# Kernel tuning notes

Measured on AMD Instinct MI355X. Metric: run time of the kernel, lower is better.

Reference implementation:

```python
import jax, jax.numpy as jnp
import numpy as np

Re = 0.001
DT = 0.01
UB = -1.0
PAD = ((0, 0), (0, 0), (1, 1), (1, 1), (1, 1))


def _conv(x, w, stride=1):
    return jax.lax.conv_general_dilated(
        x, w, (stride, stride, stride), 'VALID',
        dimension_numbers=('NCDHW', 'OIDHW', 'NCDHW'))


def _pad_zero(x):
    return jnp.pad(x, PAD)


def _pad_edge(x):
    return jnp.pad(x, PAD, mode='edge')


def bc_u(u):
    # zero halo everywhere, inlet value ub on the low-x face
    return _pad_zero(u).at[..., 0].set(UB)


bc_v = _pad_zero
bc_w = _pad_zero
bc_p = _pad_edge   # Neumann (replicate) for pressure
bc_k = _pad_edge
bc_cw = _pad_zero  # Dirichlet-0 for coarse corrections


def prol(x):
    # nearest-neighbor upsample x2 in z, y, x
    x = jnp.repeat(x, 2, axis=2)
    x = jnp.repeat(x, 2, axis=3)
    return jnp.repeat(x, 2, axis=4)


def solid_body(u, v, w, sigma):
    s = 1.0 + DT * sigma
    return u / s, v / s, w / s


def pg_vector(uu, vv, ww, u, v, w, w_diff):
    # k fields are ones; padded versions go through BC
    one = jnp.ones_like(u)
    k_uu = bc_k(one)
    k_u = 0.5 * (one * _conv(uu, w_diff) + _conv(uu * k_uu, w_diff) - u * _conv(k_uu, w_diff))
    k_v = 0.5 * (one * _conv(vv, w_diff) + _conv(vv * k_uu, w_diff) - v * _conv(k_uu, w_diff))
    k_w = 0.5 * (one * _conv(ww, w_diff) + _conv(ww * k_uu, w_diff) - w * _conv(k_uu, w_diff))
    return k_u, k_v, k_w


def f_cycle_mg(uu, vv, ww, p, pp, wA, w_x, w_y, w_z, w_res, iteration, nlevel):
    diag = wA[0, 0, 1, 1, 1]
    b = -(_conv(uu, w_x) + _conv(vv, w_y) + _conv(ww, w_z)) / DT
    nz, ny, nx = p.shape[2:]
    f = 2 ** (nlevel - 2)  # coarsening factor of the coarsest level
    for _ in range(iteration):
        w = jnp.zeros((1, 1, nz // f, ny // f, nx // f), dtype=p.dtype)
        r = _conv(pp, wA) - b
        r_s = [r]
        for _i in range(1, nlevel - 1):
            r = _conv(r, w_res, stride=2)
            r_s.append(r)
        for i in reversed(range(1, nlevel - 1)):
            ww_pad = bc_cw(w)
            w = w - _conv(ww_pad, wA) / diag + r_s[i] / diag
            w = prol(w)
        p = p - w
        p = p - _conv(pp, wA) / diag + b / diag
        pp = bc_p(p)
    return p, w, r


def reference(values_u, values_v, values_w, values_p, sigma,
              wA, w_diff, w_x, w_y, w_z, w_res, iteration, nlevel):
    u, v, w, p = values_u, values_v, values_w, values_p
    u, v, w = solid_body(u, v, w, sigma)
    uu, vv, ww, pp = bc_u(u), bc_v(v), bc_w(w), bc_p(p)

    k_u, k_v, k_w = pg_vector(uu, vv, ww, u, v, w, w_diff)
    b_u = u + 0.5 * (Re * k_u * DT - u * _conv(uu, w_x) * DT - v * _conv(uu, w_y) * DT - w * _conv(uu, w_z) * DT) - _conv(pp, w_x) * DT
    b_v = v + 0.5 * (Re * k_v * DT - u * _conv(vv, w_x) * DT - v * _conv(vv, w_y) * DT - w * _conv(vv, w_z) * DT) - _conv(pp, w_y) * DT
    b_w = w + 0.5 * (Re * k_w * DT - u * _conv(ww, w_x) * DT - v * _conv(ww, w_y) * DT - w * _conv(ww, w_z) * DT) - _conv(pp, w_z) * DT
    b_u, b_v, b_w = solid_body(b_u, b_v, b_w, sigma)
    b_uu, b_vv, b_ww = bc_u(b_u), bc_v(b_v), bc_w(b_w)

    k_u, k_v, k_w = pg_vector(b_uu, b_vv, b_ww, b_u, b_v, b_w, w_diff)
    u = u + Re * k_u * DT - b_u * _conv(b_uu, w_x) * DT - b_v * _conv(b_uu, w_y) * DT - b_w * _conv(b_uu, w_z) * DT - _conv(pp, w_x) * DT
    v = v + Re * k_v * DT - b_u * _conv(b_vv, w_x) * DT - b_v * _conv(b_vv, w_y) * DT - b_w * _conv(b_vv, w_z) * DT - _conv(pp, w_y) * DT
    w = w + Re * k_w * DT - b_u * _conv(b_ww, w_x) * DT - b_v * _conv(b_ww, w_y) * DT - b_w * _conv(b_ww, w_z) * DT - _conv(pp, w_z) * DT
    u, v, w = solid_body(u, v, w, sigma)
    uu, vv, ww = bc_u(u), bc_v(v), bc_w(w)

    p, w_mg, r = f_cycle_mg(uu, vv, ww, p, pp, wA, w_x, w_y, w_z, w_res, iteration, nlevel)
    pp = bc_p(p)
    u = u - _conv(pp, w_x) * DT
    v = v - _conv(pp, w_y) * DT
    w = w - _conv(pp, w_z) * DT
    u, v, w = solid_body(u, v, w, sigma)
    return u, v, w, p, w_mg, r


def setup_inputs() -> dict:
    key = jax.random.key(0)
    ks = jax.random.split(key, 5)
    NZ, NY, NX = 64, 128, 256
    shape = (1, 1, NZ, NY, NX)

    # 7-point Laplacian for A and diff
    lap = np.zeros((1, 1, 3, 3, 3), np.float32)
    lap[0, 0, 1, 1, 1] = -6.0
    for d, i in [(2, 0), (2, 2), (3, 0), (3, 2), (4, 0), (4, 2)]:
        idx = [0, 0, 1, 1, 1]
        idx[d] = i
        lap[tuple(idx)] = 1.0
    # central differences
    wx = np.zeros((1, 1, 3, 3, 3), np.float32); wx[0, 0, 1, 1, 0] = -0.5; wx[0, 0, 1, 1, 2] = 0.5
    wy = np.zeros((1, 1, 3, 3, 3), np.float32); wy[0, 0, 1, 0, 1] = -0.5; wy[0, 0, 1, 2, 1] = 0.5
    wz = np.zeros((1, 1, 3, 3, 3), np.float32); wz[0, 0, 0, 1, 1] = -0.5; wz[0, 0, 2, 1, 1] = 0.5
    wres = np.full((1, 1, 2, 2, 2), 0.125, np.float32)

    return {
        'values_u': 0.1 * jax.random.normal(ks[0], shape, jnp.float32),
        'values_v': 0.1 * jax.random.normal(ks[1], shape, jnp.float32),
        'values_w': 0.1 * jax.random.normal(ks[2], shape, jnp.float32),
        'values_p': 0.1 * jax.random.normal(ks[3], shape, jnp.float32),
        'sigma': jax.random.uniform(ks[4], shape, jnp.float32),
        'wA': jnp.asarray(lap),
        'w_diff': jnp.asarray(lap),
        'w_x': jnp.asarray(wx),
        'w_y': jnp.asarray(wy),
        'w_z': jnp.asarray(wz),
        'w_res': jnp.asarray(wres),
        'iteration': 2,
        'nlevel': 6,
    }
```

## Files before the change

### kernel.cpp

```cpp
#include <hip/hip_runtime.h>


constexpr int NZ = 64, NY = 128, NX = 256;
constexpr int NTOT = NZ * NY * NX;
constexpr float DT  = 0.01f;
constexpr float RE  = 0.001f;
constexpr float UBC = -1.0f;
constexpr float DIAG = -6.0f;
constexpr float SIXTH = 1.0f / 6.0f;

__device__ __forceinline__ int idx3(int z, int y, int x) {
    return (z * NY + y) * NX + x;
}

union F4 { float4 v; float f[4]; };

__device__ __forceinline__ float4 ld4(const float* __restrict__ f, int z, int y, int x0) {
    return *reinterpret_cast<const float4*>(&f[idx3(z, y, x0)]);
}
__device__ __forceinline__ void st4(float* __restrict__ f, int c, const F4& a) {
    *reinterpret_cast<float4*>(&f[c]) = a.v;
}

__device__ __forceinline__ void row0(const float* __restrict__ f, int z, int y, int x0,
                                     bool ok, float o[4]) {
    if (ok) { F4 a; a.v = ld4(f, z, y, x0);
        #pragma unroll
        for (int i = 0; i < 4; i++) o[i] = a.f[i];
    } else {
        #pragma unroll
        for (int i = 0; i < 4; i++) o[i] = 0.f;
    }
}
__device__ __forceinline__ void row3s(const float* __restrict__ u, const float* __restrict__ v,
                                      const float* __restrict__ w, const float* __restrict__ sg,
                                      int z, int y, int x0, bool ok,
                                      float uo[4], float vo[4], float wo[4]) {
    if (ok) {
        F4 a, b, c, s;
        a.v = ld4(u, z, y, x0); b.v = ld4(v, z, y, x0);
        c.v = ld4(w, z, y, x0); s.v = ld4(sg, z, y, x0);
        #pragma unroll
        for (int i = 0; i < 4; i++) {
            float iv = 1.f / (1.f + DT * s.f[i]);
            uo[i] = a.f[i] * iv; vo[i] = b.f[i] * iv; wo[i] = c.f[i] * iv;
        }
    } else {
        #pragma unroll
        for (int i = 0; i < 4; i++) { uo[i] = vo[i] = wo[i] = 0.f; }
    }
}

__device__ __forceinline__ float ld_p_s(const float* __restrict__ f, int z, int y, int x) {
    x = x < 0 ? 0 : (x > NX - 1 ? NX - 1 : x);
    y = y < 0 ? 0 : (y > NY - 1 ? NY - 1 : y);
    z = z < 0 ? 0 : (z > NZ - 1 ? NZ - 1 : z);
    return f[idx3(z, y, x)];
}

__global__ __launch_bounds__(256) void k_predict(
    const float* __restrict__ u, const float* __restrict__ v, const float* __restrict__ w,
    const float* __restrict__ p, const float* __restrict__ sg,
    float* __restrict__ bu, float* __restrict__ bv, float* __restrict__ bw) {
    int tx = threadIdx.x, y = blockIdx.x * 4 + threadIdx.y, z = blockIdx.y;
    int x0 = tx << 2, c = idx3(z, y, x0);

    F4 sc; sc.v = ld4(sg, z, y, x0);
    F4 u4, v4, w4; u4.v = ld4(u, z, y, x0); v4.v = ld4(v, z, y, x0); w4.v = ld4(w, z, y, x0);
    float inv[4], uc[4], vc[4], wc[4];
    #pragma unroll
    for (int i = 0; i < 4; i++) {
        inv[i] = 1.f / (1.f + DT * sc.f[i]);
        uc[i] = u4.f[i] * inv[i]; vc[i] = v4.f[i] * inv[i]; wc[i] = w4.f[i] * inv[i];
    }
    float uym[4], vym[4], wym[4], uyp[4], vyp[4], wyp[4];
    float uzm[4], vzm[4], wzm[4], uzp[4], vzp[4], wzp[4];
    row3s(u, v, w, sg, z, y - 1, x0, y > 0,      uym, vym, wym);
    row3s(u, v, w, sg, z, y + 1, x0, y < NY - 1, uyp, vyp, wyp);
    row3s(u, v, w, sg, z - 1, y, x0, z > 0,      uzm, vzm, wzm);
    row3s(u, v, w, sg, z + 1, y, x0, z < NZ - 1, uzp, vzp, wzp);

    float uxmS, vxmS, wxmS, uxpS, vxpS, wxpS;
    if (tx > 0) { float iv = 1.f / (1.f + DT * sg[c - 1]);
        uxmS = u[c - 1] * iv; vxmS = v[c - 1] * iv; wxmS = w[c - 1] * iv; }
    else { uxmS = UBC; vxmS = 0.f; wxmS = 0.f; }
    if (tx < 63) { float iv = 1.f / (1.f + DT * sg[c + 4]);
        uxpS = u[c + 4] * iv; vxpS = v[c + 4] * iv; wxpS = w[c + 4] * iv; }
    else { uxpS = vxpS = wxpS = 0.f; }

    F4 pc, pym, pyp, pzm, pzp;
    pc.v  = ld4(p, z, y, x0);
    pym.v = ld4(p, z, y > 0 ? y - 1 : 0, x0);
    pyp.v = ld4(p, z, y < NY - 1 ? y + 1 : y, x0);
    pzm.v = ld4(p, z > 0 ? z - 1 : 0, y, x0);
    pzp.v = ld4(p, z < NZ - 1 ? z + 1 : z, y, x0);
    float pxmS = tx ? p[c - 1] : pc.f[0];
    float pxpS = (tx < 63) ? p[c + 4] : pc.f[3];

    F4 obu, obv, obw;
    #pragma unroll
    for (int i = 0; i < 4; i++) {
        float uxm = i ? uc[i - 1] : uxmS, uxp = (i < 3) ? uc[i + 1] : uxpS;
        float vxm = i ? vc[i - 1] : vxmS, vxp = (i < 3) ? vc[i + 1] : vxpS;
        float wxm = i ? wc[i - 1] : wxmS, wxp = (i < 3) ? wc[i + 1] : wxpS;
        float pxm = i ? pc.f[i - 1] : pxmS, pxp = (i < 3) ? pc.f[i + 1] : pxpS;
        float dpx = 0.5f * (pxp - pxm);
        float dpy = 0.5f * (pyp.f[i] - pym.f[i]);
        float dpz = 0.5f * (pzp.f[i] - pzm.f[i]);
        float lap_u = uxm + uxp + uym[i] + uyp[i] + uzm[i] + uzp[i] - 6.f * uc[i];
        float lap_v = vxm + vxp + vym[i] + vyp[i] + vzm[i] + vzp[i] - 6.f * vc[i];
        float lap_w = wxm + wxp + wym[i] + wyp[i] + wzm[i] + wzp[i] - 6.f * wc[i];
        float bun = uc[i] + 0.5f * (RE * lap_u * DT
                    - uc[i] * (0.5f * (uxp - uxm)) * DT
                    - vc[i] * (0.5f * (uyp[i] - uym[i])) * DT
                    - wc[i] * (0.5f * (uzp[i] - uzm[i])) * DT) - dpx * DT;
        float bvn = vc[i] + 0.5f * (RE * lap_v * DT
                    - uc[i] * (0.5f * (vxp - vxm)) * DT
                    - vc[i] * (0.5f * (vyp[i] - vym[i])) * DT
                    - wc[i] * (0.5f * (vzp[i] - vzm[i])) * DT) - dpy * DT;
        float bwn = wc[i] + 0.5f * (RE * lap_w * DT
                    - uc[i] * (0.5f * (wxp - wxm)) * DT
                    - vc[i] * (0.5f * (wyp[i] - wym[i])) * DT
                    - wc[i] * (0.5f * (wzp[i] - wzm[i])) * DT) - dpz * DT;
        obu.f[i] = bun * inv[i];
        obv.f[i] = bvn * inv[i];
        obw.f[i] = bwn * inv[i];
    }
    st4(bu, c, obu); st4(bv, c, obv); st4(bw, c, obw);
}

__global__ __launch_bounds__(256) void k_correct(
    const float* __restrict__ u, const float* __restrict__ v, const float* __restrict__ w,
    const float* __restrict__ sg,
    const float* __restrict__ bu, const float* __restrict__ bv, const float* __restrict__ bw,
    const float* __restrict__ p,
    float* __restrict__ u2, float* __restrict__ v2, float* __restrict__ w2) {
    int tx = threadIdx.x, y = blockIdx.x * 4 + threadIdx.y, z = blockIdx.y;
    int x0 = tx << 2, c = idx3(z, y, x0);

    F4 sc; sc.v = ld4(sg, z, y, x0);
    F4 u4, v4, w4; u4.v = ld4(u, z, y, x0); v4.v = ld4(v, z, y, x0); w4.v = ld4(w, z, y, x0);
    F4 buc, bvc, bwc; buc.v = ld4(bu, z, y, x0); bvc.v = ld4(bv, z, y, x0); bwc.v = ld4(bw, z, y, x0);

    float uym[4], vym[4], wym[4], uyp[4], vyp[4], wyp[4];
    float uzm[4], vzm[4], wzm[4], uzp[4], vzp[4], wzp[4];
    row0(bu, z, y - 1, x0, y > 0, uym);      row0(bv, z, y - 1, x0, y > 0, vym);
    row0(bw, z, y - 1, x0, y > 0, wym);
    row0(bu, z, y + 1, x0, y < NY - 1, uyp); row0(bv, z, y + 1, x0, y < NY - 1, vyp);
    row0(bw, z, y + 1, x0, y < NY - 1, wyp);
    row0(bu, z - 1, y, x0, z > 0, uzm);      row0(bv, z - 1, y, x0, z > 0, vzm);
    row0(bw, z - 1, y, x0, z > 0, wzm);
    row0(bu, z + 1, y, x0, z < NZ - 1, uzp); row0(bv, z + 1, y, x0, z < NZ - 1, vzp);
    row0(bw, z + 1, y, x0, z < NZ - 1, wzp);

    float uxmS = tx ? bu[c - 1] : UBC,  uxpS = (tx < 63) ? bu[c + 4] : 0.f;
    float vxmS = tx ? bv[c - 1] : 0.f,  vxpS = (tx < 63) ? bv[c + 4] : 0.f;
    float wxmS = tx ? bw[c - 1] : 0.f,  wxpS = (tx < 63) ? bw[c + 4] : 0.f;

    F4 pc, pym, pyp, pzm, pzp;
    pc.v  = ld4(p, z, y, x0);
    pym.v = ld4(p, z, y > 0 ? y - 1 : 0, x0);
    pyp.v = ld4(p, z, y < NY - 1 ? y + 1 : y, x0);
    pzm.v = ld4(p, z > 0 ? z - 1 : 0, y, x0);
    pzp.v = ld4(p, z < NZ - 1 ? z + 1 : z, y, x0);
    float pxmS = tx ? p[c - 1] : pc.f[0];
    float pxpS = (tx < 63) ? p[c + 4] : pc.f[3];

    F4 ou, ov, ow;
    #pragma unroll
    for (int i = 0; i < 4; i++) {
        float inv = 1.f / (1.f + DT * sc.f[i]);
        float u1c = u4.f[i] * inv, v1c = v4.f[i] * inv, w1c = w4.f[i] * inv;
        float uxm = i ? buc.f[i - 1] : uxmS, uxp = (i < 3) ? buc.f[i + 1] : uxpS;
        float vxm = i ? bvc.f[i - 1] : vxmS, vxp = (i < 3) ? bvc.f[i + 1] : vxpS;
        float wxm = i ? bwc.f[i - 1] : wxmS, wxp = (i < 3) ? bwc.f[i + 1] : wxpS;
        float pxm = i ? pc.f[i - 1] : pxmS, pxp = (i < 3) ? pc.f[i + 1] : pxpS;
        float dpx = 0.5f * (pxp - pxm);
        float dpy = 0.5f * (pyp.f[i] - pym.f[i]);
        float dpz = 0.5f * (pzp.f[i] - pzm.f[i]);
        float lap_u = uxm + uxp + uym[i] + uyp[i] + uzm[i] + uzp[i] - 6.f * buc.f[i];
        float lap_v = vxm + vxp + vym[i] + vyp[i] + vzm[i] + vzp[i] - 6.f * bvc.f[i];
        float lap_w = wxm + wxp + wym[i] + wyp[i] + wzm[i] + wzp[i] - 6.f * bwc.f[i];
        float un = u1c + RE * lap_u * DT
                   - buc.f[i] * (0.5f * (uxp - uxm)) * DT
                   - bvc.f[i] * (0.5f * (uyp[i] - uym[i])) * DT
                   - bwc.f[i] * (0.5f * (uzp[i] - uzm[i])) * DT - dpx * DT;
        float vn = v1c + RE * lap_v * DT
                   - buc.f[i] * (0.5f * (vxp - vxm)) * DT
                   - bvc.f[i] * (0.5f * (vyp[i] - vym[i])) * DT
                   - bwc.f[i] * (0.5f * (vzp[i] - vzm[i])) * DT - dpy * DT;
        float wn = w1c + RE * lap_w * DT
                   - buc.f[i] * (0.5f * (wxp - wxm)) * DT
                   - bvc.f[i] * (0.5f * (wyp[i] - wym[i])) * DT
                   - bwc.f[i] * (0.5f * (wzp[i] - wzm[i])) * DT - dpz * DT;
        ou.f[i] = un * inv; ov.f[i] = vn * inv; ow.f[i] = wn * inv;
    }
    st4(u2, c, ou); st4(v2, c, ov); st4(w2, c, ow);
}

__global__ __launch_bounds__(256) void k_divresid(
    const float* __restrict__ u2, const float* __restrict__ v2, const float* __restrict__ w2,
    const float* __restrict__ p, float* __restrict__ r0) {
    int tx = threadIdx.x, y = blockIdx.x * 4 + threadIdx.y, z = blockIdx.y;
    int x0 = tx << 2, c = idx3(z, y, x0);

    F4 uc; uc.v = ld4(u2, z, y, x0);
    float uxmS = tx ? u2[c - 1] : UBC, uxpS = (tx < 63) ? u2[c + 4] : 0.f;
    float vym[4], vyp[4], wzm[4], wzp[4];
    row0(v2, z, y - 1, x0, y > 0, vym);
    row0(v2, z, y + 1, x0, y < NY - 1, vyp);
    row0(w2, z - 1, y, x0, z > 0, wzm);
    row0(w2, z + 1, y, x0, z < NZ - 1, wzp);

    F4 pc, pym, pyp, pzm, pzp;
    pc.v  = ld4(p, z, y, x0);
    pym.v = ld4(p, z, y > 0 ? y - 1 : 0, x0);
    pyp.v = ld4(p, z, y < NY - 1 ? y + 1 : y, x0);
    pzm.v = ld4(p, z > 0 ? z - 1 : 0, y, x0);
    pzp.v = ld4(p, z < NZ - 1 ? z + 1 : z, y, x0);
    float pxmS = tx ? p[c - 1] : pc.f[0];
    float pxpS = (tx < 63) ? p[c + 4] : pc.f[3];

    F4 o;
    #pragma unroll
    for (int i = 0; i < 4; i++) {
        float uxm = i ? uc.f[i - 1] : uxmS, uxp = (i < 3) ? uc.f[i + 1] : uxpS;
        float bval = -(0.5f * (uxp - uxm) + 0.5f * (vyp[i] - vym[i])
                       + 0.5f * (wzp[i] - wzm[i])) / DT;
        float pxm = i ? pc.f[i - 1] : pxmS, pxp = (i < 3) ? pc.f[i + 1] : pxpS;
        float lap = pxm + pxp + pym.f[i] + pyp.f[i] + pzm.f[i] + pzp.f[i] - 6.f * pc.f[i];
        o.f[i] = lap - bval;
    }
    st4(r0, c, o);
}

__global__ __launch_bounds__(512) void k_rescdown(const float* __restrict__ rf,
    float* __restrict__ r1, float* __restrict__ r2, float* __restrict__ r3,
    float* __restrict__ r4) {
    __shared__ float l1[8][16][32];
    __shared__ float l2[4][8][16];
    __shared__ float l3[2][4][8];
    int tid = threadIdx.x;
    int bx = blockIdx.x, by = blockIdx.y, bz = blockIdx.z;
    int lx = tid & 31, ly = (tid >> 5) & 15;
    int x1 = bx * 32 + lx, y1 = by * 16 + ly;
    #pragma unroll
    for (int lz = 0; lz < 8; lz++) {
        int z1 = bz * 8 + lz;
        const float* b0 = &rf[idx3(2 * z1, 2 * y1, 2 * x1)];
        float2 a  = *reinterpret_cast<const float2*>(b0);
        float2 bq = *reinterpret_cast<const float2*>(b0 + NX);
        float2 cq = *reinterpret_cast<const float2*>(b0 + NY * NX);
        float2 dq = *reinterpret_cast<const float2*>(b0 + NY * NX + NX);
        float val = 0.125f * (a.x + a.y + bq.x + bq.y + cq.x + cq.y + dq.x + dq.y);
        l1[lz][ly][lx] = val;
        r1[((z1 * 64) + y1) * 128 + x1] = val;
    }
    __syncthreads();
    {
        int tx2 = tid & 15, ty2 = (tid >> 4) & 7, tz2 = tid >> 7;
        float s = l1[2*tz2][2*ty2][2*tx2]     + l1[2*tz2][2*ty2][2*tx2+1]
                + l1[2*tz2][2*ty2+1][2*tx2]   + l1[2*tz2][2*ty2+1][2*tx2+1]
                + l1[2*tz2+1][2*ty2][2*tx2]   + l1[2*tz2+1][2*ty2][2*tx2+1]
                + l1[2*tz2+1][2*ty2+1][2*tx2] + l1[2*tz2+1][2*ty2+1][2*tx2+1];
        float val = 0.125f * s;
        l2[tz2][ty2][tx2] = val;
        int x2 = bx * 16 + tx2, y2 = by * 8 + ty2, z2 = bz * 4 + tz2;
        r2[((z2 * 32) + y2) * 64 + x2] = val;
    }
    __syncthreads();
    if (tid < 64) {
        int tx3 = tid & 7, ty3 = (tid >> 3) & 3, tz3 = tid >> 5;
        float s = l2[2*tz3][2*ty3][2*tx3]     + l2[2*tz3][2*ty3][2*tx3+1]
                + l2[2*tz3][2*ty3+1][2*tx3]   + l2[2*tz3][2*ty3+1][2*tx3+1]
                + l2[2*tz3+1][2*ty3][2*tx3]   + l2[2*tz3+1][2*ty3][2*tx3+1]
                + l2[2*tz3+1][2*ty3+1][2*tx3] + l2[2*tz3+1][2*ty3+1][2*tx3+1];
        float val = 0.125f * s;
        l3[tz3][ty3][tx3] = val;
        int x3 = bx * 8 + tx3, y3 = by * 4 + ty3, z3 = bz * 2 + tz3;
        r3[((z3 * 16) + y3) * 32 + x3] = val;
    }
    __syncthreads();
    if (tid < 8) {
        int tx4 = tid & 3, ty4 = tid >> 2;
        float s = l3[0][2*ty4][2*tx4]   + l3[0][2*ty4][2*tx4+1]
                + l3[0][2*ty4+1][2*tx4] + l3[0][2*ty4+1][2*tx4+1]
                + l3[1][2*ty4][2*tx4]   + l3[1][2*ty4][2*tx4+1]
                + l3[1][2*ty4+1][2*tx4] + l3[1][2*ty4+1][2*tx4+1];
        int x4 = bx * 4 + tx4, y4 = by * 2 + ty4, z4 = bz;
        r4[((z4 * 8) + y4) * 16 + x4] = 0.125f * s;
    }
}

__device__ __forceinline__ float a4p(const float* __restrict__ r4, int z3, int y3, int x3) {
    if ((unsigned)z3 >= 8u || (unsigned)y3 >= 16u || (unsigned)x3 >= 32u) return 0.f;
    return r4[(((z3 >> 1) * 8) + (y3 >> 1)) * 16 + (x3 >> 1)] / DIAG;
}

__global__ __launch_bounds__(512) void k_cup(const float* __restrict__ r4,
    const float* __restrict__ r3, const float* __restrict__ r2, float* __restrict__ C) {
    __shared__ float Bl[4][6][10];
    int tid = threadIdx.x;
    int bx = blockIdx.x, by = blockIdx.y, bz = blockIdx.z;
    int Bz0 = bz * 2 - 1, By0 = by * 4 - 1, Bx0 = bx * 8 - 1;
    if (tid < 240) {
        int lx = tid % 10, ly = (tid / 10) % 6, lz = tid / 60;
        int z3 = Bz0 + lz, y3 = By0 + ly, x3 = Bx0 + lx;
        float val = 0.f;
        if ((unsigned)z3 < 8u && (unsigned)y3 < 16u && (unsigned)x3 < 32u) {
            float wcn = r4[(((z3 >> 1) * 8) + (y3 >> 1)) * 16 + (x3 >> 1)] / DIAG;
            float lap = a4p(r4, z3 - 1, y3, x3) + a4p(r4, z3 + 1, y3, x3)
                      + a4p(r4, z3, y3 - 1, x3) + a4p(r4, z3, y3 + 1, x3)
                      + a4p(r4, z3, y3, x3 - 1) + a4p(r4, z3, y3, x3 + 1) - 6.f * wcn;
            val = wcn - lap / DIAG + r3[((z3 * 16) + y3) * 32 + x3] / DIAG;
        }
        Bl[lz][ly][lx] = val;
    }
    __syncthreads();
    int tx = tid & 15, ty = (tid >> 4) & 7, tz = tid >> 7;
    int x2 = bx * 16 + tx, y2 = by * 8 + ty, z2 = bz * 4 + tz;
    auto bl = [&](int z, int y, int x) -> float {
        if ((unsigned)z >= 16u || (unsigned)y >= 32u || (unsigned)x >= 64u) return 0.f;
        return Bl[(z >> 1) - Bz0][(y >> 1) - By0][(x >> 1) - Bx0];
    };
    float wB = Bl[(z2 >> 1) - Bz0][(y2 >> 1) - By0][(x2 >> 1) - Bx0];
    float lap = bl(z2 - 1, y2, x2) + bl(z2 + 1, y2, x2)
              + bl(z2, y2 - 1, x2) + bl(z2, y2 + 1, x2)
              + bl(z2, y2, x2 - 1) + bl(z2, y2, x2 + 1) - 6.f * wB;
    int i = ((z2 * 32) + y2) * 64 + x2;
    C[i] = wB - lap / DIAG + r2[i] / DIAG;
}

__device__ __forceinline__ float wprol(const float* __restrict__ Wc,
                                       int zz, int yy, int xx, int Z, int Y, int X) {
    if ((unsigned)xx >= (unsigned)X || (unsigned)yy >= (unsigned)Y || (unsigned)zz >= (unsigned)Z) return 0.f;
    return Wc[(((zz >> 1) * (Y >> 1)) + (yy >> 1)) * (X >> 1) + (xx >> 1)];
}
__global__ void k_up(const float* __restrict__ Wc, const float* __restrict__ r,
                     float* __restrict__ out) {
    int X = blockDim.x, Y = gridDim.x, Z = gridDim.y;
    int x = threadIdx.x, y = blockIdx.x, z = blockIdx.y;
    float wcn = Wc[(((z >> 1) * (Y >> 1)) + (y >> 1)) * (X >> 1) + (x >> 1)];
    float lap = wprol(Wc, z - 1, y, x, Z, Y, X) + wprol(Wc, z + 1, y, x, Z, Y, X)
              + wprol(Wc, z, y - 1, x, Z, Y, X) + wprol(Wc, z, y + 1, x, Z, Y, X)
              + wprol(Wc, z, y, x - 1, Z, Y, X) + wprol(Wc, z, y, x + 1, Z, Y, X)
              - 6.f * wcn;
    int i = (z * Y + y) * X + x;
    out[i] = wcn - lap / DIAG + r[i] / DIAG;
}

__global__ __launch_bounds__(256) void k_pup_resid(
    const float* __restrict__ pin, const float* __restrict__ D0,
    const float* __restrict__ r0, float* __restrict__ p1, float* __restrict__ r1res) {
    int tx = threadIdx.x, y = blockIdx.x * 4 + threadIdx.y, z = blockIdx.y;
    int x0 = tx << 2, c = idx3(z, y, x0);
    int cz = z >> 1, cy = y >> 1, cx0 = tx << 1;

    const float* Drow = &D0[(cz * 64 + cy) * 128];
    float cr[4];
    cr[1] = Drow[cx0]; cr[2] = Drow[cx0 + 1];
    cr[0] = tx ? Drow[cx0 - 1] : cr[1];
    cr[3] = (tx < 63) ? Drow[cx0 + 2] : cr[2];
    int cym = y ? (y - 1) >> 1 : 0, cyp = (y < NY - 1) ? (y + 1) >> 1 : cy;
    int czm = z ? (z - 1) >> 1 : 0, czp = (z < NZ - 1) ? (z + 1) >> 1 : cz;
    float2 dym = *reinterpret_cast<const float2*>(&D0[(cz * 64 + cym) * 128 + cx0]);
    float2 dyp = *reinterpret_cast<const float2*>(&D0[(cz * 64 + cyp) * 128 + cx0]);
    float2 dzm = *reinterpret_cast<const float2*>(&D0[(czm * 64 + cy) * 128 + cx0]);
    float2 dzp = *reinterpret_cast<const float2*>(&D0[(czp * 64 + cy) * 128 + cx0]);

    F4 rc, rym, ryp, rzm, rzp, pin4;
    rc.v  = ld4(r0, z, y, x0);
    rym.v = ld4(r0, z, y > 0 ? y - 1 : 0, x0);
    ryp.v = ld4(r0, z, y < NY - 1 ? y + 1 : y, x0);
    rzm.v = ld4(r0, z > 0 ? z - 1 : 0, y, x0);
    rzp.v = ld4(r0, z < NZ - 1 ? z + 1 : z, y, x0);
    pin4.v = ld4(pin, z, y, x0);
    float rxmS = tx ? r0[c - 1] : rc.f[0];
    float rxpS = (tx < 63) ? r0[c + 4] : rc.f[3];

    F4 op1, ores;
    #pragma unroll
    for (int i = 0; i < 4; i++) {
        float Dc  = cr[1 + (i >> 1)];
        float Dxm = (i == 0) ? cr[0] : cr[1 + ((i - 1) >> 1)];
        float Dxp = (i == 3) ? cr[3] : cr[1 + ((i + 1) >> 1)];
        float Dym = (i < 2) ? dym.x : dym.y;
        float Dyp = (i < 2) ? dyp.x : dyp.y;
        float Dzm = (i < 2) ? dzm.x : dzm.y;
        float Dzp = (i < 2) ? dzp.x : dzp.y;
        float lapD = Dxm + Dxp + Dym + Dyp + Dzm + Dzp - 6.f * Dc;
        float rxm = i ? rc.f[i - 1] : rxmS, rxp = (i < 3) ? rc.f[i + 1] : rxpS;
        float lapR = rxm + rxp + rym.f[i] + ryp.f[i] + rzm.f[i] + rzp.f[i] - 6.f * rc.f[i];
        op1.f[i]  = pin4.f[i] - Dc + rc.f[i] * SIXTH;
        ores.f[i] = rc.f[i] - lapD + lapR * SIXTH;
    }
    st4(p1, c, op1); st4(r1res, c, ores);
}

__global__ __launch_bounds__(256) void k_pup2(
    const float* __restrict__ D1, const float* __restrict__ r1res,
    float* __restrict__ pIO, float* __restrict__ wmg) {
    int tx = threadIdx.x, y = blockIdx.x * 4 + threadIdx.y, z = blockIdx.y;
    int x0 = tx << 2, c = idx3(z, y, x0);
    int cz = z >> 1, cy = y >> 1, cx0 = tx << 1;
    float2 d2 = *reinterpret_cast<const float2*>(&D1[(cz * 64 + cy) * 128 + cx0]);
    F4 rr, pp; rr.v = ld4(r1res, z, y, x0); pp.v = ld4(pIO, z, y, x0);
    F4 op, ow;
    #pragma unroll
    for (int i = 0; i < 4; i++) {
        float wv = (i < 2) ? d2.x : d2.y;
        op.f[i] = pp.f[i] - wv + rr.f[i] * SIXTH;
        ow.f[i] = wv;
    }
    st4(pIO, c, op); st4(wmg, c, ow);
}

__global__ __launch_bounds__(256) void k_final(
    const float* __restrict__ p,
    const float* __restrict__ u2, const float* __restrict__ v2, const float* __restrict__ w2,
    const float* __restrict__ sg,
    float* __restrict__ uo, float* __restrict__ vo, float* __restrict__ wo) {
    int tx = threadIdx.x, y = blockIdx.x * 4 + threadIdx.y, z = blockIdx.y;
    int x0 = tx << 2, c = idx3(z, y, x0);
    F4 pc, pym, pyp, pzm, pzp;
    pc.v  = ld4(p, z, y, x0);
    pym.v = ld4(p, z, y > 0 ? y - 1 : 0, x0);
    pyp.v = ld4(p, z, y < NY - 1 ? y + 1 : y, x0);
    pzm.v = ld4(p, z > 0 ? z - 1 : 0, y, x0);
    pzp.v = ld4(p, z < NZ - 1 ? z + 1 : z, y, x0);
    float pxmS = tx ? p[c - 1] : pc.f[0];
    float pxpS = (tx < 63) ? p[c + 4] : pc.f[3];
    F4 sc; sc.v = ld4(sg, z, y, x0);
    F4 a, b, cc; a.v = ld4(u2, z, y, x0); b.v = ld4(v2, z, y, x0); cc.v = ld4(w2, z, y, x0);
    F4 ou, ov, ow;
    #pragma unroll
    for (int i = 0; i < 4; i++) {
        float pxm = i ? pc.f[i - 1] : pxmS, pxp = (i < 3) ? pc.f[i + 1] : pxpS;
        float inv = 1.f / (1.f + DT * sc.f[i]);
        ou.f[i] = (a.f[i]  - 0.5f * (pxp - pxm) * DT) * inv;
        ov.f[i] = (b.f[i]  - 0.5f * (pyp.f[i] - pym.f[i]) * DT) * inv;
        ow.f[i] = (cc.f[i] - 0.5f * (pzp.f[i] - pzm.f[i]) * DT) * inv;
    }
    st4(uo, c, ou); st4(vo, c, ov); st4(wo, c, ow);
}

extern "C" void kernel_launch(void* const* d_in, const int* in_sizes, int n_in,
                              void* d_out, int out_size, void* d_ws, size_t ws_size,
                              hipStream_t stream) {
    const float* in_u  = (const float*)d_in[0];
    const float* in_v  = (const float*)d_in[1];
    const float* in_w  = (const float*)d_in[2];
    const float* in_p  = (const float*)d_in[3];
    const float* in_sg = (const float*)d_in[4];

    float* out   = (float*)d_out;
    float* O_u   = out;
    float* O_v   = out + (size_t)NTOT;
    float* O_w   = out + (size_t)2 * NTOT;
    float* O_p   = out + (size_t)3 * NTOT;
    float* O_wmg = out + (size_t)4 * NTOT;
    float* O_r   = out + (size_t)5 * NTOT;

    float* ws  = (float*)d_ws;
    float* A0  = ws;
    float* A1  = ws + (size_t)NTOT;
    float* A2  = ws + (size_t)2 * NTOT;
    float* r1  = ws + (size_t)3 * NTOT;
    float* r2  = r1 + 262144;
    float* r3  = r2 + 32768;
    float* r4w = r3 + 4096;
    float* Cw  = r4w + 512;
    float* Dw  = Cw + 32768;

    dim3 gF(NY / 4, NZ);
    dim3 bF(64, 4);
    dim3 gC(4, 4, 4);

    k_predict  <<<gF, bF, 0, stream>>>(in_u, in_v, in_w, in_p, in_sg, O_u, O_v, O_w);
    k_correct  <<<gF, bF, 0, stream>>>(in_u, in_v, in_w, in_sg, O_u, O_v, O_w, in_p, A0, A1, A2);
    k_divresid <<<gF, bF, 0, stream>>>(A0, A1, A2, in_p, O_wmg );

    k_rescdown <<<gC, dim3(512), 0, stream>>>(O_wmg, r1, r2, r3, r4w);
    k_cup      <<<gC, dim3(512), 0, stream>>>(r4w, r3, r2, Cw);
    k_up       <<<dim3(64, 32), dim3(128), 0, stream>>>(Cw, r1, Dw);
    k_pup_resid<<<gF, bF, 0, stream>>>(in_p, Dw, O_wmg, O_p , O_u );

    k_rescdown <<<gC, dim3(512), 0, stream>>>(O_u, r1, r2, r3, O_r);
    k_cup      <<<gC, dim3(512), 0, stream>>>(O_r, r3, r2, Cw);
    k_up       <<<dim3(64, 32), dim3(128), 0, stream>>>(Cw, r1, Dw);
    k_pup2     <<<gF, bF, 0, stream>>>(Dw, O_u , O_p , O_wmg );

    k_final    <<<gF, bF, 0, stream>>>(O_p, A0, A1, A2, in_sg, O_u, O_v, O_w);
}
```

Baseline: 101.9 us.

## Fuse predictor into corrector, restriction into residual kernels, merge coarse up-sweeps

Predictor and corrector become one kernel that recomputes the predicted velocity for the center and its six neighbour rows instead of writing and rereading it, with the x-edge neighbours handled per point. The first restriction level moves into the residual kernels through a shared-memory 2x2x2 average, and the two coarse up-sweep kernels merge into one that holds the intermediate level in shared memory. This cuts kernel launches and full-grid memory traffic, at the price of redundant predictor arithmetic and many extra neighbour loads in the fused momentum kernel.

New measurement: 191.7 us. 1.88x slower.

```diff
diff --git a/kernel.cpp b/kernel.cpp
--- a/kernel.cpp
+++ b/kernel.cpp
@@ -22,14 +22,18 @@
     *reinterpret_cast<float4*>(&f[c]) = a.v;
 }
 
+__device__ __forceinline__ void zero4(float o[4]) {
+    #pragma unroll
+    for (int i = 0; i < 4; i++) o[i] = 0.f;
+}
+
 __device__ __forceinline__ void row0(const float* __restrict__ f, int z, int y, int x0,
                                      bool ok, float o[4]) {
     if (ok) { F4 a; a.v = ld4(f, z, y, x0);
         #pragma unroll
         for (int i = 0; i < 4; i++) o[i] = a.f[i];
     } else {
-        #pragma unroll
-        for (int i = 0; i < 4; i++) o[i] = 0.f;
+        zero4(o);
     }
 }
 __device__ __forceinline__ void row3s(const float* __restrict__ u, const float* __restrict__ v,
@@ -46,25 +50,15 @@
             uo[i] = a.f[i] * iv; vo[i] = b.f[i] * iv; wo[i] = c.f[i] * iv;
         }
     } else {
-        #pragma unroll
-        for (int i = 0; i < 4; i++) { uo[i] = vo[i] = wo[i] = 0.f; }
-    }
-}
-
-__device__ __forceinline__ float ld_p_s(const float* __restrict__ f, int z, int y, int x) {
-    x = x < 0 ? 0 : (x > NX - 1 ? NX - 1 : x);
-    y = y < 0 ? 0 : (y > NY - 1 ? NY - 1 : y);
-    z = z < 0 ? 0 : (z > NZ - 1 ? NZ - 1 : z);
-    return f[idx3(z, y, x)];
-}
-
-__global__ __launch_bounds__(256) void k_predict(
+        zero4(uo); zero4(vo); zero4(wo);
+    }
+}
+
+__device__ __forceinline__ void bu_row4(
     const float* __restrict__ u, const float* __restrict__ v, const float* __restrict__ w,
     const float* __restrict__ p, const float* __restrict__ sg,
-    float* __restrict__ bu, float* __restrict__ bv, float* __restrict__ bw) {
-    int tx = threadIdx.x, y = blockIdx.x * 4 + threadIdx.y, z = blockIdx.y;
+    int z, int y, int tx, float obu[4], float obv[4], float obw[4]) {
     int x0 = tx << 2, c = idx3(z, y, x0);
-
     F4 sc; sc.v = ld4(sg, z, y, x0);
     F4 u4, v4, w4; u4.v = ld4(u, z, y, x0); v4.v = ld4(v, z, y, x0); w4.v = ld4(w, z, y, x0);
     float inv[4], uc[4], vc[4], wc[4];
@@ -97,7 +91,6 @@
     float pxmS = tx ? p[c - 1] : pc.f[0];
     float pxpS = (tx < 63) ? p[c + 4] : pc.f[3];
 
-    F4 obu, obv, obw;
     #pragma unroll
     for (int i = 0; i < 4; i++) {
         float uxm = i ? uc[i - 1] : uxmS, uxp = (i < 3) ? uc[i + 1] : uxpS;
@@ -122,41 +115,79 @@
                     - uc[i] * (0.5f * (wxp - wxm)) * DT
                     - vc[i] * (0.5f * (wyp[i] - wym[i])) * DT
                     - wc[i] * (0.5f * (wzp[i] - wzm[i])) * DT) - dpz * DT;
-        obu.f[i] = bun * inv[i];
-        obv.f[i] = bvn * inv[i];
-        obw.f[i] = bwn * inv[i];
-    }
-    st4(bu, c, obu); st4(bv, c, obv); st4(bw, c, obw);
-}
-
-__global__ __launch_bounds__(256) void k_correct(
+        obu[i] = bun * inv[i];
+        obv[i] = bvn * inv[i];
+        obw[i] = bwn * inv[i];
+    }
+}
+
+__device__ __forceinline__ void bu_point(
     const float* __restrict__ u, const float* __restrict__ v, const float* __restrict__ w,
-    const float* __restrict__ sg,
-    const float* __restrict__ bu, const float* __restrict__ bv, const float* __restrict__ bw,
-    const float* __restrict__ p,
+    const float* __restrict__ p, const float* __restrict__ sg,
+    int z, int y, int x, float& rbu, float& rbv, float& rbw) {
+    int c = idx3(z, y, x);
+    float inv = 1.f / (1.f + DT * sg[c]);
+    float uc = u[c] * inv, vc = v[c] * inv, wc = w[c] * inv;
+    float uxm, vxm, wxm, uxp, vxp, wxp, uym, vym, wym, uyp, vyp, wyp;
+    float uzm, vzm, wzm, uzp, vzp, wzp;
+    if (x > 0) { int i = c - 1; float iv = 1.f / (1.f + DT * sg[i]);
+        uxm = u[i]*iv; vxm = v[i]*iv; wxm = w[i]*iv; } else { uxm = UBC; vxm = wxm = 0.f; }
+    if (x < NX - 1) { int i = c + 1; float iv = 1.f / (1.f + DT * sg[i]);
+        uxp = u[i]*iv; vxp = v[i]*iv; wxp = w[i]*iv; } else { uxp = vxp = wxp = 0.f; }
+    if (y > 0) { int i = c - NX; float iv = 1.f / (1.f + DT * sg[i]);
+        uym = u[i]*iv; vym = v[i]*iv; wym = w[i]*iv; } else { uym = vym = wym = 0.f; }
+    if (y < NY - 1) { int i = c + NX; float iv = 1.f / (1.f + DT * sg[i]);
+        uyp = u[i]*iv; vyp = v[i]*iv; wyp = w[i]*iv; } else { uyp = vyp = wyp = 0.f; }
+    if (z > 0) { int i = c - NX*NY; float iv = 1.f / (1.f + DT * sg[i]);
+        uzm = u[i]*iv; vzm = v[i]*iv; wzm = w[i]*iv; } else { uzm = vzm = wzm = 0.f; }
+    if (z < NZ - 1) { int i = c + NX*NY; float iv = 1.f / (1.f + DT * sg[i]);
+        uzp = u[i]*iv; vzp = v[i]*iv; wzp = w[i]*iv; } else { uzp = vzp = wzp = 0.f; }
+    float pxm = x > 0 ? p[c - 1] : p[c];
+    float pxp = x < NX - 1 ? p[c + 1] : p[c];
+    float pym = y > 0 ? p[c - NX] : p[c];
+    float pyp = y < NY - 1 ? p[c + NX] : p[c];
+    float pzm = z > 0 ? p[c - NX*NY] : p[c];
+    float pzp = z < NZ - 1 ? p[c + NX*NY] : p[c];
+    float dpx = 0.5f * (pxp - pxm), dpy = 0.5f * (pyp - pym), dpz = 0.5f * (pzp - pzm);
+    float lap_u = uxm + uxp + uym + uyp + uzm + uzp - 6.f * uc;
+    float lap_v = vxm + vxp + vym + vyp + vzm + vzp - 6.f * vc;
+    float lap_w = wxm + wxp + wym + wyp + wzm + wzp - 6.f * wc;
+    rbu = (uc + 0.5f * (RE * lap_u * DT - uc * (0.5f * (uxp - uxm)) * DT
+          - vc * (0.5f * (uyp - uym)) * DT - wc * (0.5f * (uzp - uzm)) * DT) - dpx * DT) * inv;
+    rbv = (vc + 0.5f * (RE * lap_v * DT - uc * (0.5f * (vxp - vxm)) * DT
+          - vc * (0.5f * (vyp - vym)) * DT - wc * (0.5f * (vzp - vzm)) * DT) - dpy * DT) * inv;
+    rbw = (wc + 0.5f * (RE * lap_w * DT - uc * (0.5f * (wxp - wxm)) * DT
+          - vc * (0.5f * (wyp - wym)) * DT - wc * (0.5f * (wzp - wzm)) * DT) - dpz * DT) * inv;
+}
+
+__global__ __launch_bounds__(256) void k_mom(
+    const float* __restrict__ u, const float* __restrict__ v, const float* __restrict__ w,
+    const float* __restrict__ sg, const float* __restrict__ p,
     float* __restrict__ u2, float* __restrict__ v2, float* __restrict__ w2) {
     int tx = threadIdx.x, y = blockIdx.x * 4 + threadIdx.y, z = blockIdx.y;
     int x0 = tx << 2, c = idx3(z, y, x0);
 
+    float buc[4], bvc[4], bwc[4];
+    float uym[4], vym[4], wym[4], uyp[4], vyp[4], wyp[4];
+    float uzm[4], vzm[4], wzm[4], uzp[4], vzp[4], wzp[4];
+    bu_row4(u, v, w, p, sg, z, y, tx, buc, bvc, bwc);
+    if (y > 0)      bu_row4(u, v, w, p, sg, z, y - 1, tx, uym, vym, wym);
+    else { zero4(uym); zero4(vym); zero4(wym); }
+    if (y < NY - 1) bu_row4(u, v, w, p, sg, z, y + 1, tx, uyp, vyp, wyp);
+    else { zero4(uyp); zero4(vyp); zero4(wyp); }
+    if (z > 0)      bu_row4(u, v, w, p, sg, z - 1, y, tx, uzm, vzm, wzm);
+    else { zero4(uzm); zero4(vzm); zero4(wzm); }
+    if (z < NZ - 1) bu_row4(u, v, w, p, sg, z + 1, y, tx, uzp, vzp, wzp);
+    else { zero4(uzp); zero4(vzp); zero4(wzp); }
+
+    float uxmS, vxmS, wxmS, uxpS, vxpS, wxpS;
+    if (tx > 0) bu_point(u, v, w, p, sg, z, y, x0 - 1, uxmS, vxmS, wxmS);
+    else { uxmS = UBC; vxmS = 0.f; wxmS = 0.f; }
+    if (tx < 63) bu_point(u, v, w, p, sg, z, y, x0 + 4, uxpS, vxpS, wxpS);
+    else { uxpS = vxpS = wxpS = 0.f; }
+
     F4 sc; sc.v = ld4(sg, z, y, x0);
     F4 u4, v4, w4; u4.v = ld4(u, z, y, x0); v4.v = ld4(v, z, y, x0); w4.v = ld4(w, z, y, x0);
-    F4 buc, bvc, bwc; buc.v = ld4(bu, z, y, x0); bvc.v = ld4(bv, z, y, x0); bwc.v = ld4(bw, z, y, x0);
-
-    float uym[4], vym[4], wym[4], uyp[4], vyp[4], wyp[4];
-    float uzm[4], vzm[4], wzm[4], uzp[4], vzp[4], wzp[4];
-    row0(bu, z, y - 1, x0, y > 0, uym);      row0(bv, z, y - 1, x0, y > 0, vym);
-    row0(bw, z, y - 1, x0, y > 0, wym);
-    row0(bu, z, y + 1, x0, y < NY - 1, uyp); row0(bv, z, y + 1, x0, y < NY - 1, vyp);
-    row0(bw, z, y + 1, x0, y < NY - 1, wyp);
-    row0(bu, z - 1, y, x0, z > 0, uzm);      row0(bv, z - 1, y, x0, z > 0, vzm);
-    row0(bw, z - 1, y, x0, z > 0, wzm);
-    row0(bu, z + 1, y, x0, z < NZ - 1, uzp); row0(bv, z + 1, y, x0, z < NZ - 1, vzp);
-    row0(bw, z + 1, y, x0, z < NZ - 1, wzp);
-
-    float uxmS = tx ? bu[c - 1] : UBC,  uxpS = (tx < 63) ? bu[c + 4] : 0.f;
-    float vxmS = tx ? bv[c - 1] : 0.f,  vxpS = (tx < 63) ? bv[c + 4] : 0.f;
-    float wxmS = tx ? bw[c - 1] : 0.f,  wxpS = (tx < 63) ? bw[c + 4] : 0.f;
-
     F4 pc, pym, pyp, pzm, pzp;
     pc.v  = ld4(p, z, y, x0);
     pym.v = ld4(p, z, y > 0 ? y - 1 : 0, x0);
@@ -171,37 +202,39 @@
     for (int i = 0; i < 4; i++) {
         float inv = 1.f / (1.f + DT * sc.f[i]);
         float u1c = u4.f[i] * inv, v1c = v4.f[i] * inv, w1c = w4.f[i] * inv;
-        float uxm = i ? buc.f[i - 1] : uxmS, uxp = (i < 3) ? buc.f[i + 1] : uxpS;
-        float vxm = i ? bvc.f[i - 1] : vxmS, vxp = (i < 3) ? bvc.f[i + 1] : vxpS;
-        float wxm = i ? bwc.f[i - 1] : wxmS, wxp = (i < 3) ? bwc.f[i + 1] : wxpS;
+        float uxm = i ? buc[i - 1] : uxmS, uxp = (i < 3) ? buc[i + 1] : uxpS;
+        float vxm = i ? bvc[i - 1] : vxmS, vxp = (i < 3) ? bvc[i + 1] : vxpS;
+        float wxm = i ? bwc[i - 1] : wxmS, wxp = (i < 3) ? bwc[i + 1] : wxpS;
         float pxm = i ? pc.f[i - 1] : pxmS, pxp = (i < 3) ? pc.f[i + 1] : pxpS;
         float dpx = 0.5f * (pxp - pxm);
         float dpy = 0.5f * (pyp.f[i] - pym.f[i]);
         float dpz = 0.5f * (pzp.f[i] - pzm.f[i]);
-        float lap_u = uxm + uxp + uym[i] + uyp[i] + uzm[i] + uzp[i] - 6.f * buc.f[i];
-        float lap_v = vxm + vxp + vym[i] + vyp[i] + vzm[i] + vzp[i] - 6.f * bvc.f[i];
-        float lap_w = wxm + wxp + wym[i] + wyp[i] + wzm[i] + wzp[i] - 6.f * bwc.f[i];
+        float lap_u = uxm + uxp + uym[i] + uyp[i] + uzm[i] + uzp[i] - 6.f * buc[i];
+        float lap_v = vxm + vxp + vym[i] + vyp[i] + vzm[i] + vzp[i] - 6.f * bvc[i];
+        float lap_w = wxm + wxp + wym[i] + wyp[i] + wzm[i] + wzp[i] - 6.f * bwc[i];
         float un = u1c + RE * lap_u * DT
-                   - buc.f[i] * (0.5f * (uxp - uxm)) * DT
-                   - bvc.f[i] * (0.5f * (uyp[i] - uym[i])) * DT
-                   - bwc.f[i] * (0.5f * (uzp[i] - uzm[i])) * DT - dpx * DT;
+                   - buc[i] * (0.5f * (uxp - uxm)) * DT
+                   - bvc[i] * (0.5f * (uyp[i] - uym[i])) * DT
+                   - bwc[i] * (0.5f * (uzp[i] - uzm[i])) * DT - dpx * DT;
         float vn = v1c + RE * lap_v * DT
-                   - buc.f[i] * (0.5f * (vxp - vxm)) * DT
-                   - bvc.f[i] * (0.5f * (vyp[i] - vym[i])) * DT
-                   - bwc.f[i] * (0.5f * (vzp[i] - vzm[i])) * DT - dpy * DT;
+                   - buc[i] * (0.5f * (vxp - vxm)) * DT
+                   - bvc[i] * (0.5f * (vyp[i] - vym[i])) * DT
+                   - bwc[i] * (0.5f * (vzp[i] - vzm[i])) * DT - dpy * DT;
         float wn = w1c + RE * lap_w * DT
-                   - buc.f[i] * (0.5f * (wxp - wxm)) * DT
-                   - bvc.f[i] * (0.5f * (wyp[i] - wym[i])) * DT
-                   - bwc.f[i] * (0.5f * (wzp[i] - wzm[i])) * DT - dpz * DT;
+                   - buc[i] * (0.5f * (wxp - wxm)) * DT
+                   - bvc[i] * (0.5f * (wyp[i] - wym[i])) * DT
+                   - bwc[i] * (0.5f * (wzp[i] - wzm[i])) * DT - dpz * DT;
         ou.f[i] = un * inv; ov.f[i] = vn * inv; ow.f[i] = wn * inv;
     }
     st4(u2, c, ou); st4(v2, c, ov); st4(w2, c, ow);
 }
 
-__global__ __launch_bounds__(256) void k_divresid(
+__global__ __launch_bounds__(512) void k_divresid_r(
     const float* __restrict__ u2, const float* __restrict__ v2, const float* __restrict__ w2,
-    const float* __restrict__ p, float* __restrict__ r0) {
-    int tx = threadIdx.x, y = blockIdx.x * 4 + threadIdx.y, z = blockIdx.y;
+    const float* __restrict__ p, float* __restrict__ r0, float* __restrict__ r1) {
+    __shared__ float lds[2][4][256];
+    int tx = threadIdx.x, ty = threadIdx.y, tz = threadIdx.z;
+    int y = blockIdx.x * 4 + ty, z = blockIdx.y * 2 + tz;
     int x0 = tx << 2, c = idx3(z, y, x0);
 
     F4 uc; uc.v = ld4(u2, z, y, x0);
@@ -232,40 +265,37 @@
         o.f[i] = lap - bval;
     }
     st4(r0, c, o);
-}
-
-__global__ __launch_bounds__(512) void k_rescdown(const float* __restrict__ rf,
-    float* __restrict__ r1, float* __restrict__ r2, float* __restrict__ r3,
-    float* __restrict__ r4) {
-    __shared__ float l1[8][16][32];
+    *reinterpret_cast<float4*>(&lds[tz][ty][x0]) = o.v;
+    __syncthreads();
+    int tid = (tz * 4 + ty) * 64 + tx;
+    if (tid < 256) {
+        int y1loc = tid >> 7, x1 = tid & 127;
+        int xf = x1 << 1, yf = y1loc << 1;
+        float s = lds[0][yf][xf]     + lds[0][yf][xf + 1]
+                + lds[0][yf + 1][xf] + lds[0][yf + 1][xf + 1]
+                + lds[1][yf][xf]     + lds[1][yf][xf + 1]
+                + lds[1][yf + 1][xf] + lds[1][yf + 1][xf + 1];
+        int y1 = blockIdx.x * 2 + y1loc, z1 = blockIdx.y;
+        r1[(z1 * 64 + y1) * 128 + x1] = 0.125f * s;
+    }
+}
+
+__global__ __launch_bounds__(512) void k_down(const float* __restrict__ r1,
+    float* __restrict__ r2, float* __restrict__ r3, float* __restrict__ r4) {
     __shared__ float l2[4][8][16];
     __shared__ float l3[2][4][8];
     int tid = threadIdx.x;
     int bx = blockIdx.x, by = blockIdx.y, bz = blockIdx.z;
-    int lx = tid & 31, ly = (tid >> 5) & 15;
-    int x1 = bx * 32 + lx, y1 = by * 16 + ly;
-    #pragma unroll
-    for (int lz = 0; lz < 8; lz++) {
-        int z1 = bz * 8 + lz;
-        const float* b0 = &rf[idx3(2 * z1, 2 * y1, 2 * x1)];
-        float2 a  = *reinterpret_cast<const float2*>(b0);
-        float2 bq = *reinterpret_cast<const float2*>(b0 + NX);
-        float2 cq = *reinterpret_cast<const float2*>(b0 + NY * NX);
-        float2 dq = *reinterpret_cast<const float2*>(b0 + NY * NX + NX);
-        float val = 0.125f * (a.x + a.y + bq.x + bq.y + cq.x + cq.y + dq.x + dq.y);
-        l1[lz][ly][lx] = val;
-        r1[((z1 * 64) + y1) * 128 + x1] = val;
-    }
-    __syncthreads();
     {
         int tx2 = tid & 15, ty2 = (tid >> 4) & 7, tz2 = tid >> 7;
-        float s = l1[2*tz2][2*ty2][2*tx2]     + l1[2*tz2][2*ty2][2*tx2+1]
-                + l1[2*tz2][2*ty2+1][2*tx2]   + l1[2*tz2][2*ty2+1][2*tx2+1]
-                + l1[2*tz2+1][2*ty2][2*tx2]   + l1[2*tz2+1][2*ty2][2*tx2+1]
-                + l1[2*tz2+1][2*ty2+1][2*tx2] + l1[2*tz2+1][2*ty2+1][2*tx2+1];
-        float val = 0.125f * s;
+        int x2 = bx * 16 + tx2, y2 = by * 8 + ty2, z2 = bz * 4 + tz2;
+        const float* b0 = &r1[((size_t)(2 * z2) * 64 + 2 * y2) * 128 + 2 * x2];
+        float2 a  = *reinterpret_cast<const float2*>(b0);
+        float2 bq = *reinterpret_cast<const float2*>(b0 + 128);
+        float2 cq = *reinterpret_cast<const float2*>(b0 + 64 * 128);
+        float2 dq = *reinterpret_cast<const float2*>(b0 + 64 * 128 + 128);
+        float val = 0.125f * (a.x + a.y + bq.x + bq.y + cq.x + cq.y + dq.x + dq.y);
         l2[tz2][ty2][tx2] = val;
-        int x2 = bx * 16 + tx2, y2 = by * 8 + ty2, z2 = bz * 4 + tz2;
         r2[((z2 * 32) + y2) * 64 + x2] = val;
     }
     __syncthreads();
@@ -297,15 +327,17 @@
     return r4[(((z3 >> 1) * 8) + (y3 >> 1)) * 16 + (x3 >> 1)] / DIAG;
 }
 
-__global__ __launch_bounds__(512) void k_cup(const float* __restrict__ r4,
-    const float* __restrict__ r3, const float* __restrict__ r2, float* __restrict__ C) {
+__global__ __launch_bounds__(512) void k_upf(const float* __restrict__ r4,
+    const float* __restrict__ r3, const float* __restrict__ r2,
+    const float* __restrict__ r1, float* __restrict__ D) {
     __shared__ float Bl[4][6][10];
+    __shared__ float Cl[6][10][18];
     int tid = threadIdx.x;
     int bx = blockIdx.x, by = blockIdx.y, bz = blockIdx.z;
-    int Bz0 = bz * 2 - 1, By0 = by * 4 - 1, Bx0 = bx * 8 - 1;
+    int B0z = bz * 2 - 1, B0y = by * 4 - 1, B0x = bx * 8 - 1;
     if (tid < 240) {
         int lx = tid % 10, ly = (tid / 10) % 6, lz = tid / 60;
-        int z3 = Bz0 + lz, y3 = By0 + ly, x3 = Bx0 + lx;
+        int z3 = B0z + lz, y3 = B0y + ly, x3 = B0x + lx;
         float val = 0.f;
         if ((unsigned)z3 < 8u && (unsigned)y3 < 16u && (unsigned)x3 < 32u) {
             float wcn = r4[(((z3 >> 1) * 8) + (y3 >> 1)) * 16 + (x3 >> 1)] / DIAG;
@@ -317,42 +349,48 @@
         Bl[lz][ly][lx] = val;
     }
     __syncthreads();
-    int tx = tid & 15, ty = (tid >> 4) & 7, tz = tid >> 7;
-    int x2 = bx * 16 + tx, y2 = by * 8 + ty, z2 = bz * 4 + tz;
-    auto bl = [&](int z, int y, int x) -> float {
-        if ((unsigned)z >= 16u || (unsigned)y >= 32u || (unsigned)x >= 64u) return 0.f;
-        return Bl[(z >> 1) - Bz0][(y >> 1) - By0][(x >> 1) - Bx0];
+    int C0z = bz * 4 - 1, C0y = by * 8 - 1, C0x = bx * 16 - 1;
+    auto pB = [&](int z2, int y2, int x2) -> float {
+        if ((unsigned)z2 >= 16u || (unsigned)y2 >= 32u || (unsigned)x2 >= 64u) return 0.f;
+        return Bl[(z2 >> 1) - B0z][(y2 >> 1) - B0y][(x2 >> 1) - B0x];
     };
-    float wB = Bl[(z2 >> 1) - Bz0][(y2 >> 1) - By0][(x2 >> 1) - Bx0];
-    float lap = bl(z2 - 1, y2, x2) + bl(z2 + 1, y2, x2)
-              + bl(z2, y2 - 1, x2) + bl(z2, y2 + 1, x2)
-              + bl(z2, y2, x2 - 1) + bl(z2, y2, x2 + 1) - 6.f * wB;
-    int i = ((z2 * 32) + y2) * 64 + x2;
-    C[i] = wB - lap / DIAG + r2[i] / DIAG;
-}
-
-__device__ __forceinline__ float wprol(const float* __restrict__ Wc,
-                                       int zz, int yy, int xx, int Z, int Y, int X) {
-    if ((unsigned)xx >= (unsigned)X || (unsigned)yy >= (unsigned)Y || (unsigned)zz >= (unsigned)Z) return 0.f;
-    return Wc[(((zz >> 1) * (Y >> 1)) + (yy >> 1)) * (X >> 1) + (xx >> 1)];
-}
-__global__ void k_up(const float* __restrict__ Wc, const float* __restrict__ r,
-                     float* __restrict__ out) {
-    int X = blockDim.x, Y = gridDim.x, Z = gridDim.y;
-    int x = threadIdx.x, y = blockIdx.x, z = blockIdx.y;
-    float wcn = Wc[(((z >> 1) * (Y >> 1)) + (y >> 1)) * (X >> 1) + (x >> 1)];
-    float lap = wprol(Wc, z - 1, y, x, Z, Y, X) + wprol(Wc, z + 1, y, x, Z, Y, X)
-              + wprol(Wc, z, y - 1, x, Z, Y, X) + wprol(Wc, z, y + 1, x, Z, Y, X)
-              + wprol(Wc, z, y, x - 1, Z, Y, X) + wprol(Wc, z, y, x + 1, Z, Y, X)
-              - 6.f * wcn;
-    int i = (z * Y + y) * X + x;
-    out[i] = wcn - lap / DIAG + r[i] / DIAG;
-}
-
-__global__ __launch_bounds__(256) void k_pup_resid(
+    for (int i = tid; i < 1080; i += 512) {
+        int lx = i % 18, ly = (i / 18) % 10, lz = i / 180;
+        int z2 = C0z + lz, y2 = C0y + ly, x2 = C0x + lx;
+        float val = 0.f;
+        if ((unsigned)z2 < 16u && (unsigned)y2 < 32u && (unsigned)x2 < 64u) {
+            float wB = Bl[(z2 >> 1) - B0z][(y2 >> 1) - B0y][(x2 >> 1) - B0x];
+            float lap = pB(z2 - 1, y2, x2) + pB(z2 + 1, y2, x2)
+                      + pB(z2, y2 - 1, x2) + pB(z2, y2 + 1, x2)
+                      + pB(z2, y2, x2 - 1) + pB(z2, y2, x2 + 1) - 6.f * wB;
+            val = wB - lap / DIAG + r2[((z2 * 32) + y2) * 64 + x2] / DIAG;
+        }
+        Cl[lz][ly][lx] = val;
+    }
+    __syncthreads();
+    auto pC = [&](int z1, int y1, int x1) -> float {
+        if ((unsigned)z1 >= 32u || (unsigned)y1 >= 64u || (unsigned)x1 >= 128u) return 0.f;
+        return Cl[(z1 >> 1) - C0z][(y1 >> 1) - C0y][(x1 >> 1) - C0x];
+    };
+    for (int i = tid; i < 4096; i += 512) {
+        int lx = i & 31, ly = (i >> 5) & 15, lz = i >> 9;
+        int z1 = bz * 8 + lz, y1 = by * 16 + ly, x1 = bx * 32 + lx;
+        float wC = Cl[(z1 >> 1) - C0z][(y1 >> 1) - C0y][(x1 >> 1) - C0x];
+        float lap = pC(z1 - 1, y1, x1) + pC(z1 + 1, y1, x1)
+                  + pC(z1, y1 - 1, x1) + pC(z1, y1 + 1, x1)
+                  + pC(z1, y1, x1 - 1) + pC(z1, y1, x1 + 1) - 6.f * wC;
+        int idx = (z1 * 64 + y1) * 128 + x1;
+        D[idx] = wC - lap / DIAG + r1[idx] / DIAG;
+    }
+}
+
+__global__ __launch_bounds__(512) void k_pup_resid_r(
     const float* __restrict__ pin, const float* __restrict__ D0,
-    const float* __restrict__ r0, float* __restrict__ p1, float* __restrict__ r1res) {
-    int tx = threadIdx.x, y = blockIdx.x * 4 + threadIdx.y, z = blockIdx.y;
+    const float* __restrict__ r0, float* __restrict__ p1, float* __restrict__ r1res,
+    float* __restrict__ r1) {
+    __shared__ float lds[2][4][256];
+    int tx = threadIdx.x, ty = threadIdx.y, tz = threadIdx.z;
+    int y = blockIdx.x * 4 + ty, z = blockIdx.y * 2 + tz;
     int x0 = tx << 2, c = idx3(z, y, x0);
     int cz = z >> 1, cy = y >> 1, cx0 = tx << 1;
 
@@ -395,6 +433,19 @@
         ores.f[i] = rc.f[i] - lapD + lapR * SIXTH;
     }
     st4(p1, c, op1); st4(r1res, c, ores);
+    *reinterpret_cast<float4*>(&lds[tz][ty][x0]) = ores.v;
+    __syncthreads();
+    int tid = (tz * 4 + ty) * 64 + tx;
+    if (tid < 256) {
+        int y1loc = tid >> 7, x1 = tid & 127;
+        int xf = x1 << 1, yf = y1loc << 1;
+        float s = lds[0][yf][xf]     + lds[0][yf][xf + 1]
+                + lds[0][yf + 1][xf] + lds[0][yf + 1][xf + 1]
+                + lds[1][yf][xf]     + lds[1][yf][xf + 1]
+                + lds[1][yf + 1][xf] + lds[1][yf + 1][xf + 1];
+        int y1 = blockIdx.x * 2 + y1loc, z1 = blockIdx.y;
+        r1[(z1 * 64 + y1) * 128 + x1] = 0.125f * s;
+    }
 }
 
 __global__ __launch_bounds__(256) void k_pup2(
@@ -469,26 +520,22 @@
     float* r2  = r1 + 262144;
     float* r3  = r2 + 32768;
     float* r4w = r3 + 4096;
-    float* Cw  = r4w + 512;
-    float* Dw  = Cw + 32768;
-
-    dim3 gF(NY / 4, NZ);
-    dim3 bF(64, 4);
+    float* Dw  = r4w + 512;
+
+    dim3 gF(NY / 4, NZ);       dim3 bF(64, 4);
+    dim3 gF2(NY / 4, NZ / 2);  dim3 bF2(64, 4, 2);
     dim3 gC(4, 4, 4);
 
-    k_predict  <<<gF, bF, 0, stream>>>(in_u, in_v, in_w, in_p, in_sg, O_u, O_v, O_w);
-    k_correct  <<<gF, bF, 0, stream>>>(in_u, in_v, in_w, in_sg, O_u, O_v, O_w, in_p, A0, A1, A2);
-    k_divresid <<<gF, bF, 0, stream>>>(A0, A1, A2, in_p, O_wmg );
-
-    k_rescdown <<<gC, dim3(512), 0, stream>>>(O_wmg, r1, r2, r3, r4w);
-    k_cup      <<<gC, dim3(512), 0, stream>>>(r4w, r3, r2, Cw);
-    k_up       <<<dim3(64, 32), dim3(128), 0, stream>>>(Cw, r1, Dw);
-    k_pup_resid<<<gF, bF, 0, stream>>>(in_p, Dw, O_wmg, O_p , O_u );
-
-    k_rescdown <<<gC, dim3(512), 0, stream>>>(O_u, r1, r2, r3, O_r);
-    k_cup      <<<gC, dim3(512), 0, stream>>>(O_r, r3, r2, Cw);
-    k_up       <<<dim3(64, 32), dim3(128), 0, stream>>>(Cw, r1, Dw);
-    k_pup2     <<<gF, bF, 0, stream>>>(Dw, O_u , O_p , O_wmg );
-
-    k_final    <<<gF, bF, 0, stream>>>(O_p, A0, A1, A2, in_sg, O_u, O_v, O_w);
-}
+    k_mom         <<<gF,  bF,  0, stream>>>(in_u, in_v, in_w, in_sg, in_p, A0, A1, A2);
+    k_divresid_r  <<<gF2, bF2, 0, stream>>>(A0, A1, A2, in_p, O_wmg , r1);
+
+    k_down        <<<gC, dim3(512), 0, stream>>>(r1, r2, r3, r4w);
+    k_upf         <<<gC, dim3(512), 0, stream>>>(r4w, r3, r2, r1, Dw);
+    k_pup_resid_r <<<gF2, bF2, 0, stream>>>(in_p, Dw, O_wmg, O_p , O_u , r1);
+
+    k_down        <<<gC, dim3(512), 0, stream>>>(r1, r2, r3, O_r);
+    k_upf         <<<gC, dim3(512), 0, stream>>>(O_r, r3, r2, r1, Dw);
+    k_pup2        <<<gF, bF, 0, stream>>>(Dw, O_u , O_p , O_wmg );
+
+    k_final       <<<gF, bF, 0, stream>>>(O_p, A0, A1, A2, in_sg, O_u, O_v, O_w);
+}
```
